# Performance work log

Measured on AMD Instinct MI355X. Metric: run time of the kernel, lower is better.

Reference implementation:

```python
import math
import jax, jax.numpy as jnp
import numpy as np

# ---- model dims ----
D = 4096          # hidden_size
N = 32            # num_attention_heads (== num_key_value_heads)
Q_LORA = 1536
KV_LORA = 512
QK_NOPE = 128
QK_ROPE = 64
QK_HEAD = QK_NOPE + QK_ROPE   # 192
V_HEAD = 128
EPS = 1e-6
T = 2048

# ---- yarn rope constants ----
ROPE_THETA = 10000.0
FACTOR = 40.0
ORIG_MAX = 4096
BETA_FAST = 32.0
BETA_SLOW = 1.0
MSCALE = 1.0
MSCALE_ALL_DIM = 1.0


def _yarn_get_mscale(scale, mscale):
    if scale <= 1.0:
        return 1.0
    return 0.1 * mscale * math.log(scale) + 1.0

# softmax scale: qk_head_dim^-0.5 * yarn_mscale^2 (rope_mscale_all_dim = 1.0)
YARN_MSCALE = _yarn_get_mscale(FACTOR, MSCALE_ALL_DIM)
SM_SCALE = QK_HEAD ** (-0.5) * YARN_MSCALE ** 2


def _yarn_cos_sin(positions):
    """DeepSeek yarn scaled rotary embeddings. positions: int [T]."""
    half = QK_ROPE // 2
    pow_ = np.arange(0, QK_ROPE, 2, dtype=np.float64) / QK_ROPE
    pos_freqs = ROPE_THETA ** pow_
    inv_extra = 1.0 / pos_freqs
    inv_inter = 1.0 / (FACTOR * pos_freqs)

    def corr_dim(n_rot):
        return (QK_ROPE * math.log(ORIG_MAX / (n_rot * 2 * math.pi))) / (2 * math.log(ROPE_THETA))

    low = max(math.floor(corr_dim(BETA_FAST)), 0)
    high = min(math.ceil(corr_dim(BETA_SLOW)), QK_ROPE - 1)
    ramp = np.clip((np.arange(half, dtype=np.float64) - low) / max(high - low, 1e-3), 0.0, 1.0)
    mask = 1.0 - ramp  # 1 where extrapolation
    inv_freq = inv_inter * (1.0 - mask) + inv_extra * mask
    inv_freq = jnp.asarray(inv_freq, jnp.float32)

    mscale_coef = _yarn_get_mscale(FACTOR, MSCALE) / _yarn_get_mscale(FACTOR, MSCALE_ALL_DIM)
    t = positions.astype(jnp.float32)
    freqs = t[:, None] * inv_freq[None, :]          # [T, half]
    return jnp.cos(freqs) * mscale_coef, jnp.sin(freqs) * mscale_coef


def _apply_rope(x_tnh, cos, sin):
    """Neox-style (split halves) rope. x: [T, N, QK_ROPE]; cos/sin: [T, half]."""
    half = QK_ROPE // 2
    x1, x2 = x_tnh[..., :half], x_tnh[..., half:]
    c, s = cos[:, None, :], sin[:, None, :]
    return jnp.concatenate([x1 * c - x2 * s, x1 * s + x2 * c], axis=-1)


def _rms_norm(x, scale, eps=EPS):
    var = jnp.mean(jnp.square(x), axis=-1, keepdims=True)
    return x * jax.lax.rsqrt(var + eps) * scale


def setup_inputs() -> dict:
    key = jax.random.key(0)
    ks = jax.random.split(key, 8)
    std = 0.02
    return {
        "x": jax.random.normal(ks[0], (T, D), jnp.float32),
        "positions": jnp.arange(T, dtype=jnp.int32),
        "w_q_down": jax.random.normal(ks[1], (D, Q_LORA), jnp.float32) * std,
        "q_norm_scale": jnp.ones((Q_LORA,), jnp.float32),
        "w_q_up": jax.random.normal(ks[2], (Q_LORA, N, QK_HEAD), jnp.float32) * std,
        "w_kv_down": jax.random.normal(ks[3], (D, KV_LORA + QK_ROPE), jnp.float32) * std,
        "kv_norm_scale": jnp.ones((KV_LORA,), jnp.float32),
        "w_kv_up": jax.random.normal(ks[4], (KV_LORA, N, QK_NOPE + V_HEAD), jnp.float32) * std,
        "w_o": jax.random.normal(ks[5], (N, V_HEAD, D), jnp.float32) * std,
    }


def reference(x, positions, w_q_down, q_norm_scale, w_q_up, w_kv_down,
              kv_norm_scale, w_kv_up, w_o):
    cos, sin = _yarn_cos_sin(positions)

    # ---- q projection (low rank) ----
    q_ta = _rms_norm(jnp.einsum('td,da->ta', x, w_q_down), q_norm_scale)
    q_tnh = jnp.einsum('ta,anh->tnh', q_ta, w_q_up)            # [T,N,192]
    q_rope = _apply_rope(q_tnh[..., QK_NOPE:], cos, sin)
    q_tnh = jnp.concatenate([q_tnh[..., :QK_NOPE], q_rope], axis=-1)

    # ---- kv projection (compressed latent) ----
    kv_sa = jnp.einsum('sd,da->sa', x, w_kv_down)              # [T, KV_LORA+64]
    k_rope = _apply_rope(kv_sa[:, None, KV_LORA:], cos, sin)   # [T,1,64]
    k_rope = jnp.broadcast_to(k_rope, (x.shape[0], N, QK_ROPE))
    kv_lat = _rms_norm(kv_sa[..., :KV_LORA], kv_norm_scale)
    kv_nope = jnp.einsum('sa,anh->snh', kv_lat, w_kv_up)       # [T,N,256]
    k_snh = jnp.concatenate([kv_nope[..., :QK_NOPE], k_rope], axis=-1)
    v_snh = kv_nope[..., QK_NOPE:]

    # ---- causal attention (prefill; padding to 128-multiple is a no-op) ----
    scores = jnp.einsum('tnh,snh->nts', q_tnh, k_snh) * SM_SCALE
    tpos = jnp.arange(x.shape[0])
    causal = tpos[:, None] >= tpos[None, :]
    scores = jnp.where(causal[None, :, :], scores, jnp.finfo(scores.dtype).min)
    probs = jax.nn.softmax(scores, axis=-1)
    out_tnh = jnp.einsum('nts,snh->tnh', probs, v_snh)

    # ---- output projection ----
    return jnp.einsum('tnh,nhd->td', out_tnh, w_o)
```

## Files before the change

### kernel.cpp

```cpp
#include <hip/hip_runtime.h>
#include <math.h>
#include <stdint.h>

#define T_    2048
#define D_    4096
#define NH_   32
#define QL_   1536
#define KVL_  512
#define ROPE_ 64
#define NOPE_ 128
#define HQK_  192
#define HV_   128
#define KVD_  576
#define NCAT_ 2112

typedef __bf16 bf16x8 __attribute__((ext_vector_type(8)));
typedef __bf16 bf16x4 __attribute__((ext_vector_type(4)));
typedef float f32x4 __attribute__((ext_vector_type(4)));

__device__ __forceinline__ void gload_lds16(const __bf16* g, __bf16* l) {
  __builtin_amdgcn_global_load_lds(
      (const __attribute__((address_space(1))) void*)g,
      (__attribute__((address_space(3))) void*)l, 16, 0, 0);
}

template <typename OutT>
__global__ __launch_bounds__(256, 3) void mfma_gemm_kernel(
    const __bf16* __restrict__ A, const __bf16* __restrict__ Bt,
    OutT* __restrict__ C, int M, int Ncols, int K) {
  __shared__ __bf16 As[128 * 32];
  __shared__ __bf16 Bs[128 * 32];
  const int tid = threadIdx.x;
  const int lane = tid & 63;
  const int w = tid >> 6;
  const int wm = w >> 1, wn = w & 1;
  const int lg = lane >> 4, lj = lane & 15;
  const int bm = blockIdx.y * 128;
  const int bn = blockIdx.x * 128;

  const int sr = lane >> 2;
  const int sc = lane & 3;
  const __bf16* ga[2]; const __bf16* gb[2];
  __bf16* la[2]; __bf16* lb[2];
  #pragma unroll
  for (int h = 0; h < 2; ++h) {
    int r = h * 64 + w * 16 + sr;
    int cg = sc ^ ((r >> 1) & 3);
    ga[h] = A  + (size_t)(bm + r) * K + cg * 8;
    gb[h] = Bt + (size_t)(bn + r) * K + cg * 8;
    la[h] = &As[(h * 64 + w * 16) * 32];
    lb[h] = &Bs[(h * 64 + w * 16) * 32];
  }

  int roa[4], rob[4];
  #pragma unroll
  for (int i = 0; i < 4; ++i) {
    int ra_ = wm * 64 + i * 16 + lj;
    roa[i] = ra_ * 32 + ((lg ^ ((ra_ >> 1) & 3)) << 3);
    int rb_ = wn * 64 + i * 16 + lj;
    rob[i] = rb_ * 32 + ((lg ^ ((rb_ >> 1) & 3)) << 3);
  }

  f32x4 acc[4][4];
  #pragma unroll
  for (int mi = 0; mi < 4; ++mi)
    #pragma unroll
    for (int ni = 0; ni < 4; ++ni) acc[mi][ni] = (f32x4){0.f, 0.f, 0.f, 0.f};

  for (int k0 = 0; k0 < K; k0 += 32) {
    __syncthreads();
    #pragma unroll
    for (int h = 0; h < 2; ++h) {
      gload_lds16(ga[h] + k0, la[h]);
      gload_lds16(gb[h] + k0, lb[h]);
    }
    __syncthreads();
    bf16x8 af[4], bfr[4];
    #pragma unroll
    for (int i = 0; i < 4; ++i) af[i]  = *(const bf16x8*)&As[roa[i]];
    #pragma unroll
    for (int i = 0; i < 4; ++i) bfr[i] = *(const bf16x8*)&Bs[rob[i]];
    #pragma unroll
    for (int mi = 0; mi < 4; ++mi)
      #pragma unroll
      for (int ni = 0; ni < 4; ++ni)
        acc[mi][ni] = __builtin_amdgcn_mfma_f32_16x16x32_bf16(af[mi], bfr[ni], acc[mi][ni], 0, 0, 0);
  }

  #pragma unroll
  for (int mi = 0; mi < 4; ++mi) {
    #pragma unroll
    for (int r = 0; r < 4; ++r) {
      int row = bm + wm * 64 + mi * 16 + lg * 4 + r;
      #pragma unroll
      for (int ni = 0; ni < 4; ++ni) {
        int col = bn + wn * 64 + ni * 16 + lj;
        if (col < Ncols) C[(size_t)row * Ncols + col] = (OutT)acc[mi][ni][r];
      }
    }
  }
}

__global__ __launch_bounds__(256) void transpose_bf16_kernel(
    const float* __restrict__ B, __bf16* __restrict__ Bt, int K, int N) {
  __shared__ float tile[64][65];
  int n0 = blockIdx.x * 64, k0 = blockIdx.y * 64;
  int tid = threadIdx.x;
  int kr = tid >> 4, nc = (tid & 15) * 4;
  #pragma unroll
  for (int i = 0; i < 4; ++i) {
    int k = kr + i * 16;
    float4 v = make_float4(0.f, 0.f, 0.f, 0.f);
    if (n0 + nc < N) v = *(const float4*)(B + (size_t)(k0 + k) * N + n0 + nc);
    tile[k][nc + 0] = v.x; tile[k][nc + 1] = v.y;
    tile[k][nc + 2] = v.z; tile[k][nc + 3] = v.w;
  }
  __syncthreads();
  int nl = tid >> 4, k4 = (tid & 15) * 4;
  #pragma unroll
  for (int i = 0; i < 4; ++i) {
    int nn = nl + i * 16;
    bf16x4 o;
    o[0] = (__bf16)tile[k4 + 0][nn]; o[1] = (__bf16)tile[k4 + 1][nn];
    o[2] = (__bf16)tile[k4 + 2][nn]; o[3] = (__bf16)tile[k4 + 3][nn];
    *(bf16x4*)(Bt + (size_t)(n0 + nn) * K + k0 + k4) = o;
  }
}

__global__ __launch_bounds__(256) void conv_bf16_kernel(
    const float* __restrict__ in, __bf16* __restrict__ out, int n8) {
  int i = blockIdx.x * 256 + threadIdx.x;
  if (i >= n8) return;
  float4 a = *(const float4*)(in + (size_t)i * 8);
  float4 b = *(const float4*)(in + (size_t)i * 8 + 4);
  bf16x8 v;
  v[0] = (__bf16)a.x; v[1] = (__bf16)a.y; v[2] = (__bf16)a.z; v[3] = (__bf16)a.w;
  v[4] = (__bf16)b.x; v[5] = (__bf16)b.y; v[6] = (__bf16)b.z; v[7] = (__bf16)b.w;
  *(bf16x8*)(out + (size_t)i * 8) = v;
}

__global__ __launch_bounds__(256) void rmsnorm_bf16_kernel(
    const float* __restrict__ in, __bf16* __restrict__ out,
    const float* __restrict__ scale, int len, int in_stride) {
  int row = blockIdx.x;
  const float* x = in + (size_t)row * in_stride;
  __bf16* y = out + (size_t)row * len;
  float ss = 0.f;
  for (int i = threadIdx.x; i < len; i += 256) { float v = x[i]; ss += v * v; }
  __shared__ float red[4];
  #pragma unroll
  for (int o = 32; o > 0; o >>= 1) ss += __shfl_down(ss, o, 64);
  int wid = threadIdx.x >> 6, lane = threadIdx.x & 63;
  if (lane == 0) red[wid] = ss;
  __syncthreads();
  if (threadIdx.x == 0) {
    float t = red[0] + red[1] + red[2] + red[3];
    red[0] = 1.0f / sqrtf(t / (float)len + 1e-6f);
  }
  __syncthreads();
  float r = red[0];
  for (int i = threadIdx.x; i < len; i += 256) y[i] = (__bf16)(x[i] * r * scale[i]);
}

struct InvFreq { float f[32]; };
__global__ __launch_bounds__(256) void rope_table_kernel(
    const int* __restrict__ pos, float* __restrict__ cosT, float* __restrict__ sinT,
    InvFreq invf) {
  int idx = blockIdx.x * 256 + threadIdx.x;
  if (idx >= T_ * 32) return;
  int t = idx >> 5, i = idx & 31;
  float fr = (float)pos[t] * invf.f[i];
  cosT[idx] = cosf(fr);
  sinT[idx] = sinf(fr);
}

__global__ __launch_bounds__(256) void rope_q_kernel(
    __bf16* __restrict__ q, const float* __restrict__ cosT, const float* __restrict__ sinT) {
  int idx = blockIdx.x * 256 + threadIdx.x;
  if (idx >= T_ * NH_ * 32) return;
  int i = idx & 31;
  int tn = idx >> 5;
  int t = tn >> 5;
  __bf16* b = q + (size_t)tn * HQK_ + NOPE_;
  float x1 = (float)b[i], x2 = (float)b[i + 32];
  float c = cosT[t * 32 + i], s = sinT[t * 32 + i];
  b[i]      = (__bf16)(x1 * c - x2 * s);
  b[i + 32] = (__bf16)(x1 * s + x2 * c);
}

__global__ __launch_bounds__(256) void rope_k_kernel(
    const float* __restrict__ src, int stride, const float* __restrict__ cosT,
    const float* __restrict__ sinT, __bf16* __restrict__ k_rope) {
  int idx = blockIdx.x * 256 + threadIdx.x;
  if (idx >= T_ * 32) return;
  int t = idx >> 5, i = idx & 31;
  const float* b = src + (size_t)t * stride;
  float x1 = b[i], x2 = b[i + 32];
  float c = cosT[idx], s = sinT[idx];
  k_rope[t * 64 + i]      = (__bf16)(x1 * c - x2 * s);
  k_rope[t * 64 + i + 32] = (__bf16)(x1 * s + x2 * c);
}

__global__ __launch_bounds__(256) void prep_vt_kernel(
    const __bf16* __restrict__ kv_nopeb, __bf16* __restrict__ Vt) {
  __shared__ __bf16 tile[64][136];
  int s0 = blockIdx.x * 64;
  int n = blockIdx.y;
  int tid = threadIdx.x;
  #pragma unroll
  for (int i = 0; i < 4; ++i) {
    int idx = tid + i * 256;
    int s = idx >> 4, c = idx & 15;
    bf16x8 v = *(const bf16x8*)(kv_nopeb + ((size_t)(s0 + s) * NH_ + n) * 256 + NOPE_ + c * 8);
    *(bf16x8*)&tile[s][c * 8] = v;
  }
  __syncthreads();
  #pragma unroll
  for (int i = 0; i < 8; ++i) {
    int idx = tid + i * 256;
    int h = idx >> 4, s4 = (idx & 15) * 4;
    bf16x4 v;
    v[0] = tile[s4 + 0][h]; v[1] = tile[s4 + 1][h];
    v[2] = tile[s4 + 2][h]; v[3] = tile[s4 + 3][h];
    *(bf16x4*)(Vt + ((size_t)n * HV_ + h) * T_ + s0 + s4) = v;
  }
}

__global__ __launch_bounds__(256) void attn_mfma_kernel(
    const __bf16* __restrict__ q_tnh, const __bf16* __restrict__ kv_nopeb,
    const __bf16* __restrict__ k_rope, const __bf16* __restrict__ Vt,
    __bf16* __restrict__ attn_out, float sm_scale) {
  __shared__ __bf16 KsL[2][24 * 32 * 8];
  __shared__ __bf16 VsL[2][4 * 128 * 8];
  __shared__ __bf16 Ps[4][16 * 64];
  const int tid = threadIdx.x;
  const int lane = tid & 63;
  const int w = tid >> 6;
  const int id = blockIdx.x;
  const int j = id >> 3;
  const int qt = 31 - (j >> 2);
  const int n = (id & 7) * 4 + (j & 3);
  const int t0 = qt * 64;
  const int lg = lane >> 4;
  const int lj = lane & 15;
  const int rowbase = t0 + w * 16;

  const __bf16* kbase[3]; size_t kstep[3]; int klds[3];
  #pragma unroll
  for (int i = 0; i < 3; ++i) {
    int task = i * 256 + tid;
    int c = task >> 5, s = task & 31;
    if (c < 16) { kbase[i] = kv_nopeb + ((size_t)s * NH_ + n) * 256 + c * 8; kstep[i] = (size_t)32 * NH_ * 256; }
    else        { kbase[i] = k_rope + (size_t)s * ROPE_ + (c - 16) * 8;      kstep[i] = (size_t)32 * ROPE_; }
    klds[i] = (i * 256 + w * 64) * 8;
  }
  const __bf16* vbase[2]; int vlds[2];
  #pragma unroll
  for (int i = 0; i < 2; ++i) {
    int task = i * 256 + tid;
    int c = task >> 7, h = task & 127;
    vbase[i] = Vt + ((size_t)n * HV_ + h) * T_ + c * 8;
    vlds[i] = (i * 256 + w * 64) * 8;
  }

  #define STAGE(tileIdx, bufIdx)                                               \
    do {                                                                       \
      __bf16* kb_ = &KsL[bufIdx][0];                                           \
      __bf16* vb_ = &VsL[bufIdx][0];                                           \
      _Pragma("unroll")                                                        \
      for (int i_ = 0; i_ < 3; ++i_)                                           \
        gload_lds16(kbase[i_] + (size_t)(tileIdx) * kstep[i_], kb_ + klds[i_]);\
      _Pragma("unroll")                                                        \
      for (int i_ = 0; i_ < 2; ++i_)                                           \
        gload_lds16(vbase[i_] + (size_t)(tileIdx) * 32, vb_ + vlds[i_]);       \
    } while (0)

  STAGE(0, 0);

  bf16x8 qf[6];
  {
    int t = t0 + w * 16 + lj;
    const __bf16* qp = q_tnh + ((size_t)t * NH_ + n) * HQK_;
    #pragma unroll
    for (int kk = 0; kk < 6; ++kk) {
      bf16x8 raw = *(const bf16x8*)(qp + kk * 32 + lg * 8);
      bf16x8 v;
      #pragma unroll
      for (int i = 0; i < 8; ++i) v[i] = (__bf16)((float)raw[i] * sm_scale);
      qf[kk] = v;
    }
  }

  f32x4 O[8];
  #pragma unroll
  for (int nb = 0; nb < 8; ++nb) O[nb] = (f32x4){0.f, 0.f, 0.f, 0.f};
  float m_r[4], l_r[4];
  #pragma unroll
  for (int r = 0; r < 4; ++r) { m_r[r] = -1e30f; l_r[r] = 0.f; }

  __syncthreads();

  const int nst = 2 * (qt + 1);
  #pragma unroll 1
  for (int st = 0; st < nst; ++st) {
    const int s0 = st * 32;
    const int cur = st & 1;
    if (st + 1 < nst) STAGE(st + 1, cur ^ 1);
    const __bf16* kb = &KsL[cur][0];
    const __bf16* vb = &VsL[cur][0];

    if (s0 <= rowbase + 15) {
      f32x4 S[2];
      #pragma unroll
      for (int sb = 0; sb < 2; ++sb) {
        f32x4 acc = (f32x4){0.f, 0.f, 0.f, 0.f};
        int srow = sb * 16 + lj;
        #pragma unroll
        for (int kk = 0; kk < 6; ++kk) {
          int c = kk * 4 + lg;
          bf16x8 b = *(const bf16x8*)&kb[(c * 32 + srow) * 8];
          acc = __builtin_amdgcn_mfma_f32_16x16x32_bf16(qf[kk], b, acc, 0, 0, 0);
        }
        S[sb] = acc;
      }
      if (s0 + 31 > rowbase) {
        #pragma unroll
        for (int sb = 0; sb < 2; ++sb)
          #pragma unroll
          for (int r = 0; r < 4; ++r) {
            int row = rowbase + lg * 4 + r;
            int col = s0 + sb * 16 + lj;
            if (col > row) S[sb][r] = -1e30f;
          }
      }
      #pragma unroll
      for (int r = 0; r < 4; ++r) {
        float mx = fmaxf(S[0][r], S[1][r]);
        mx = fmaxf(mx, __shfl_xor(mx, 1));
        mx = fmaxf(mx, __shfl_xor(mx, 2));
        mx = fmaxf(mx, __shfl_xor(mx, 4));
        mx = fmaxf(mx, __shfl_xor(mx, 8));
        float mnew = fmaxf(m_r[r], mx);
        float corr = __expf(m_r[r] - mnew);
        m_r[r] = mnew;
        float psum = 0.f;
        #pragma unroll
        for (int sb = 0; sb < 2; ++sb) {
          float pp = __expf(S[sb][r] - mnew);
          S[sb][r] = pp;
          psum += pp;
        }
        psum += __shfl_xor(psum, 1);
        psum += __shfl_xor(psum, 2);
        psum += __shfl_xor(psum, 4);
        psum += __shfl_xor(psum, 8);
        l_r[r] = l_r[r] * corr + psum;
        #pragma unroll
        for (int nb = 0; nb < 8; ++nb) O[nb][r] = O[nb][r] * corr;
      }
      #pragma unroll
      for (int sb = 0; sb < 2; ++sb) {
        int sl = sb * 16 + lj;
        int c = sl >> 3;
        #pragma unroll
        for (int r = 0; r < 4; ++r) {
          int rw = lg * 4 + r;
          Ps[w][rw * 64 + ((c ^ (rw & 7)) << 3) + (sl & 7)] = (__bf16)S[sb][r];
        }
      }
      {
        bf16x8 pa = *(const bf16x8*)&Ps[w][lj * 64 + ((lg ^ (lj & 7)) << 3)];
        #pragma unroll
        for (int nb = 0; nb < 8; ++nb) {
          int h = nb * 16 + lj;
          bf16x8 bv = *(const bf16x8*)&vb[(lg * 128 + h) * 8];
          O[nb] = __builtin_amdgcn_mfma_f32_16x16x32_bf16(pa, bv, O[nb], 0, 0, 0);
        }
      }
    }
    __syncthreads();
  }

  #pragma unroll
  for (int r = 0; r < 4; ++r) {
    float inv = 1.0f / l_r[r];
    int t = t0 + w * 16 + lg * 4 + r;
    __bf16* dst = attn_out + ((size_t)t * NH_ + n) * HV_;
    #pragma unroll
    for (int nb = 0; nb < 8; ++nb) dst[nb * 16 + lj] = (__bf16)(O[nb][r] * inv);
  }
  #undef STAGE
}

static void compute_inv_freq(float* out) {
  const double theta = 10000.0, factor = 40.0;
  const double PI = 3.14159265358979323846;
  const int rot = ROPE_;
  double low_d  = rot * log(4096.0 / (32.0 * 2.0 * PI)) / (2.0 * log(theta));
  double high_d = rot * log(4096.0 / ( 1.0 * 2.0 * PI)) / (2.0 * log(theta));
  double low = floor(low_d);  if (low < 0) low = 0;
  double high = ceil(high_d); if (high > rot - 1) high = rot - 1;
  for (int i = 0; i < 32; ++i) {
    double pf = pow(theta, (2.0 * i) / (double)rot);
    double inv_extra = 1.0 / pf;
    double inv_inter = 1.0 / (factor * pf);
    double ramp = ((double)i - low) / fmax(high - low, 0.001);
    ramp = fmin(fmax(ramp, 0.0), 1.0);
    double mask = 1.0 - ramp;
    out[i] = (float)(inv_inter * (1.0 - mask) + inv_extra * mask);
  }
}

extern "C" void kernel_launch(void* const* d_in, const int* in_sizes, int n_in,
                              void* d_out, int out_size, void* d_ws, size_t ws_size,
                              hipStream_t stream) {
  const float* x            = (const float*)d_in[0];
  const int*   positions    = (const int*)d_in[1];
  const float* w_q_down     = (const float*)d_in[2];
  const float* q_norm_scale = (const float*)d_in[3];
  const float* w_q_up       = (const float*)d_in[4];
  const float* w_kv_down    = (const float*)d_in[5];
  const float* kv_norm_scale= (const float*)d_in[6];
  const float* w_kv_up      = (const float*)d_in[7];
  const float* w_o          = (const float*)d_in[8];
  float* out = (float*)d_out;

  float* ws = (float*)d_ws;
  float*  cosT     = ws;
  float*  sinT     = ws + 65536;
  float*  cat      = ws + 131072;
  __bf16* xb       = (__bf16*)(ws + 4456448);
  __bf16* Bt_cat   = (__bf16*)(ws + 8650752);
  __bf16* Bt_qu    = (__bf16*)(ws + 13107200);
  __bf16* Bt_kvu   = (__bf16*)(ws + 17825792);
  __bf16* q_tab    = (__bf16*)(ws + 19922944);
  __bf16* kv_latb  = (__bf16*)(ws + 21495808);
  __bf16* k_ropeb  = (__bf16*)(ws + 22020096);
  __bf16* q_tnhb   = (__bf16*)(ws + 22085632);
  __bf16* kv_nopeb = (__bf16*)(ws + 28377088);
  __bf16* Vt       = (__bf16*)(ws + 13107200);
  __bf16* attn_ob  = (__bf16*)(ws + 17825792);
  __bf16* Bt_o     = (__bf16*)(ws + 4456448);
  (void)ws_size; (void)n_in; (void)in_sizes; (void)out_size;

  InvFreq invf;
  compute_inv_freq(invf.f);
  double ym = 0.1 * log(40.0) + 1.0;
  float sm_scale = (float)(ym * ym / sqrt((double)HQK_));

  rope_table_kernel<<<(T_ * 32 + 255) / 256, 256, 0, stream>>>(positions, cosT, sinT, invf);
  conv_bf16_kernel<<<T_ * D_ / 8 / 256, 256, 0, stream>>>(x, xb, T_ * D_ / 8);
  transpose_bf16_kernel<<<dim3(QL_ / 64, D_ / 64), 256, 0, stream>>>(w_q_down, Bt_cat, D_, QL_);
  transpose_bf16_kernel<<<dim3(KVD_ / 64, D_ / 64), 256, 0, stream>>>(w_kv_down, Bt_cat + (size_t)QL_ * D_, D_, KVD_);
  transpose_bf16_kernel<<<dim3(NH_ * HQK_ / 64, QL_ / 64), 256, 0, stream>>>(w_q_up, Bt_qu, QL_, NH_ * HQK_);
  transpose_bf16_kernel<<<dim3(NH_ * 256 / 64, KVL_ / 64), 256, 0, stream>>>(w_kv_up, Bt_kvu, KVL_, NH_ * 256);

  mfma_gemm_kernel<float><<<dim3((NCAT_ + 127) / 128, T_ / 128), 256, 0, stream>>>(xb, Bt_cat, cat, T_, NCAT_, D_);

  rmsnorm_bf16_kernel<<<T_, 256, 0, stream>>>(cat, q_tab, q_norm_scale, QL_, NCAT_);
  mfma_gemm_kernel<__bf16><<<dim3(NH_ * HQK_ / 128, T_ / 128), 256, 0, stream>>>(q_tab, Bt_qu, q_tnhb, T_, NH_ * HQK_, QL_);
  rope_q_kernel<<<(T_ * NH_ * 32 + 255) / 256, 256, 0, stream>>>(q_tnhb, cosT, sinT);

  rmsnorm_bf16_kernel<<<T_, 256, 0, stream>>>(cat + QL_, kv_latb, kv_norm_scale, KVL_, NCAT_);
  rope_k_kernel<<<(T_ * 32 + 255) / 256, 256, 0, stream>>>(cat + QL_ + KVL_, NCAT_, cosT, sinT, k_ropeb);
  mfma_gemm_kernel<__bf16><<<dim3(NH_ * 256 / 128, T_ / 128), 256, 0, stream>>>(kv_latb, Bt_kvu, kv_nopeb, T_, NH_ * 256, KVL_);

  prep_vt_kernel<<<dim3(T_ / 64, NH_), 256, 0, stream>>>(kv_nopeb, Vt);
  attn_mfma_kernel<<<1024, 256, 0, stream>>>(q_tnhb, kv_nopeb, k_ropeb, Vt, attn_ob, sm_scale);

  transpose_bf16_kernel<<<dim3(D_ / 64, NH_ * HV_ / 64), 256, 0, stream>>>(w_o, Bt_o, NH_ * HV_, D_);
  mfma_gemm_kernel<float><<<dim3(D_ / 128, T_ / 128), 256, 0, stream>>>(attn_ob, Bt_o, out, T_, D_, NH_ * HV_);
}
```

Measured before the change: 479.2 us.

## Double GEMM K-tile, defer softmax row-sum reduction, add MFMA priority hints

The GEMM kernel now stages a K=64 slice per iteration (doubling LDS tiles) with a new 8-way XOR swizzle, halving the number of barrier pairs per K sweep. In attention, the per-step cross-lane reduction of the softmax partial sum is dropped: each lane accumulates its own partial l, which is rescaled by the shared correction and reduced once at the end. s_setprio hints are also wrapped around the MFMA blocks to favour matrix issue. The larger LDS footprint may reduce occupancy at the 3-blocks-per-CU launch bound.

```diff
diff --git a/kernel.cpp b/kernel.cpp
--- a/kernel.cpp
+++ b/kernel.cpp
@@ -28,8 +28,8 @@
 __global__ __launch_bounds__(256, 3) void mfma_gemm_kernel(
     const __bf16* __restrict__ A, const __bf16* __restrict__ Bt,
     OutT* __restrict__ C, int M, int Ncols, int K) {
-  __shared__ __bf16 As[128 * 32];
-  __shared__ __bf16 Bs[128 * 32];
+  __shared__ __bf16 As[128 * 64];
+  __shared__ __bf16 Bs[128 * 64];
   const int tid = threadIdx.x;
   const int lane = tid & 63;
   const int w = tid >> 6;
@@ -38,27 +38,16 @@
   const int bm = blockIdx.y * 128;
   const int bn = blockIdx.x * 128;
 
-  const int sr = lane >> 2;
-  const int sc = lane & 3;
-  const __bf16* ga[2]; const __bf16* gb[2];
-  __bf16* la[2]; __bf16* lb[2];
-  #pragma unroll
-  for (int h = 0; h < 2; ++h) {
-    int r = h * 64 + w * 16 + sr;
-    int cg = sc ^ ((r >> 1) & 3);
-    ga[h] = A  + (size_t)(bm + r) * K + cg * 8;
-    gb[h] = Bt + (size_t)(bn + r) * K + cg * 8;
-    la[h] = &As[(h * 64 + w * 16) * 32];
-    lb[h] = &Bs[(h * 64 + w * 16) * 32];
-  }
-
-  int roa[4], rob[4];
+  const __bf16* ga[4]; const __bf16* gb[4];
+  int ldsoff[4];
   #pragma unroll
   for (int i = 0; i < 4; ++i) {
-    int ra_ = wm * 64 + i * 16 + lj;
-    roa[i] = ra_ * 32 + ((lg ^ ((ra_ >> 1) & 3)) << 3);
-    int rb_ = wn * 64 + i * 16 + lj;
-    rob[i] = rb_ * 32 + ((lg ^ ((rb_ >> 1) & 3)) << 3);
+    int task = i * 256 + tid;
+    int r = task >> 3, cl = task & 7;
+    int cg = cl ^ (r & 7);
+    ga[i] = A  + (size_t)(bm + r) * K + cg * 8;
+    gb[i] = Bt + (size_t)(bn + r) * K + cg * 8;
+    ldsoff[i] = (i * 256 + w * 64) * 8;
   }
 
   f32x4 acc[4][4];
@@ -67,24 +56,32 @@
     #pragma unroll
     for (int ni = 0; ni < 4; ++ni) acc[mi][ni] = (f32x4){0.f, 0.f, 0.f, 0.f};
 
-  for (int k0 = 0; k0 < K; k0 += 32) {
+  for (int k0 = 0; k0 < K; k0 += 64) {
     __syncthreads();
     #pragma unroll
-    for (int h = 0; h < 2; ++h) {
-      gload_lds16(ga[h] + k0, la[h]);
-      gload_lds16(gb[h] + k0, lb[h]);
+    for (int i = 0; i < 4; ++i) gload_lds16(ga[i] + k0, &As[ldsoff[i]]);
+    #pragma unroll
+    for (int i = 0; i < 4; ++i) gload_lds16(gb[i] + k0, &Bs[ldsoff[i]]);
+    __syncthreads();
+    #pragma unroll
+    for (int kh = 0; kh < 2; ++kh) {
+      bf16x8 af[4], bfr[4];
+      #pragma unroll
+      for (int i = 0; i < 4; ++i) {
+        int ra = wm * 64 + i * 16 + lj;
+        af[i] = *(const bf16x8*)&As[ra * 64 + ((((kh << 2) + lg) ^ (ra & 7)) << 3)];
+      }
+      #pragma unroll
+      for (int i = 0; i < 4; ++i) {
+        int rb = wn * 64 + i * 16 + lj;
+        bfr[i] = *(const bf16x8*)&Bs[rb * 64 + ((((kh << 2) + lg) ^ (rb & 7)) << 3)];
+      }
+      #pragma unroll
+      for (int mi = 0; mi < 4; ++mi)
+        #pragma unroll
+        for (int ni = 0; ni < 4; ++ni)
+          acc[mi][ni] = __builtin_amdgcn_mfma_f32_16x16x32_bf16(af[mi], bfr[ni], acc[mi][ni], 0, 0, 0);
     }
-    __syncthreads();
-    bf16x8 af[4], bfr[4];
-    #pragma unroll
-    for (int i = 0; i < 4; ++i) af[i]  = *(const bf16x8*)&As[roa[i]];
-    #pragma unroll
-    for (int i = 0; i < 4; ++i) bfr[i] = *(const bf16x8*)&Bs[rob[i]];
-    #pragma unroll
-    for (int mi = 0; mi < 4; ++mi)
-      #pragma unroll
-      for (int ni = 0; ni < 4; ++ni)
-        acc[mi][ni] = __builtin_amdgcn_mfma_f32_16x16x32_bf16(af[mi], bfr[ni], acc[mi][ni], 0, 0, 0);
   }
 
   #pragma unroll
@@ -311,6 +308,7 @@
 
     if (s0 <= rowbase + 15) {
       f32x4 S[2];
+      __builtin_amdgcn_s_setprio(1);
       #pragma unroll
       for (int sb = 0; sb < 2; ++sb) {
         f32x4 acc = (f32x4){0.f, 0.f, 0.f, 0.f};
@@ -323,6 +321,7 @@
         }
         S[sb] = acc;
       }
+      __builtin_amdgcn_s_setprio(0);
       if (s0 + 31 > rowbase) {
         #pragma unroll
         for (int sb = 0; sb < 2; ++sb)
@@ -350,10 +349,6 @@
           S[sb][r] = pp;
           psum += pp;
         }
-        psum += __shfl_xor(psum, 1);
-        psum += __shfl_xor(psum, 2);
-        psum += __shfl_xor(psum, 4);
-        psum += __shfl_xor(psum, 8);
         l_r[r] = l_r[r] * corr + psum;
         #pragma unroll
         for (int nb = 0; nb < 8; ++nb) O[nb][r] = O[nb][r] * corr;
@@ -370,12 +365,14 @@
       }
       {
         bf16x8 pa = *(const bf16x8*)&Ps[w][lj * 64 + ((lg ^ (lj & 7)) << 3)];
+        __builtin_amdgcn_s_setprio(1);
         #pragma unroll
         for (int nb = 0; nb < 8; ++nb) {
           int h = nb * 16 + lj;
           bf16x8 bv = *(const bf16x8*)&vb[(lg * 128 + h) * 8];
           O[nb] = __builtin_amdgcn_mfma_f32_16x16x32_bf16(pa, bv, O[nb], 0, 0, 0);
         }
+        __builtin_amdgcn_s_setprio(0);
       }
     }
     __syncthreads();
@@ -383,7 +380,12 @@
 
   #pragma unroll
   for (int r = 0; r < 4; ++r) {
-    float inv = 1.0f / l_r[r];
+    float lsum = l_r[r];
+    lsum += __shfl_xor(lsum, 1);
+    lsum += __shfl_xor(lsum, 2);
+    lsum += __shfl_xor(lsum, 4);
+    lsum += __shfl_xor(lsum, 8);
+    float inv = 1.0f / lsum;
     int t = t0 + w * 16 + lg * 4 + r;
     __bf16* dst = attn_out + ((size_t)t * NH_ + n) * HV_;
     #pragma unroll
```

Result: faster. 428.1 us (-10.7%).
